# Performance work log

Measured on AMD Instinct MI355X. Metric: run time of the kernel, lower is better.

Reference implementation:

```python
import jax, jax.numpy as jnp
import numpy as np

N = 8192      # nodes
NIN = 128     # input feature dim
NH = 128      # hidden dim
NC = 8        # communities
CS = N // NC  # community size


def setup_inputs() -> dict:
    key = jax.random.key(0)
    k = jax.random.split(key, 6)
    seq1 = jax.random.normal(k[0], (1, N, NIN), jnp.float32)
    seq2 = jax.random.normal(k[1], (1, N, NIN), jnp.float32)
    # dense row-stochastic-ish adjacency so GCN activations stay O(1)
    adj = jax.random.uniform(k[2], (1, N, N), jnp.float32) * (2.0 / N)
    cc_label = jnp.arange(N, dtype=jnp.int32).reshape(NC, CS)  # partition of nodes
    W = jax.random.normal(k[3], (NIN, NH), jnp.float32) / np.float32(np.sqrt(NIN))
    b = jnp.zeros((NH,), jnp.float32)
    Wb = jax.random.normal(k[4], (NH, NH), jnp.float32) / np.float32(np.sqrt(NH))
    bb = jnp.zeros((), jnp.float32)
    return {"seq1": seq1, "seq2": seq2, "adj": adj, "cc_label": cc_label,
            "W": W, "b": b, "Wb": Wb, "bb": bb}


def reference(seq1, seq2, adj, cc_label, W, b, Wb, bb):
    def gcn(seq):
        fts = jnp.einsum('bnd,dh->bnh', seq, W)            # linear
        agg = jnp.einsum('bnm,bmh->bnh', adj, fts) + b     # neighborhood aggregation
        return jax.nn.relu(agg)

    h1 = gcn(seq1)[0]   # [N, NH]
    h2 = gcn(seq2)[0]   # [N, NH]

    # ragged per-community gather (communities are equal-size here)
    hg1 = h1[cc_label]  # [NC, CS, NH]
    hg2 = h2[cc_label]  # [NC, CS, NH]

    # AvgReadout (msk=None) + sigmoid -> per-community summary
    c = jax.nn.sigmoid(jnp.mean(hg1, axis=1))              # [NC, NH]

    # Discriminator: bilinear f_k(h, c) = h @ Wb @ c + bb
    cw = jnp.einsum('hk,nk->nh', Wb, c)                    # [NC, NH]
    sc1 = jnp.einsum('nch,nh->nc', hg1, cw) + bb           # [NC, CS]
    sc2 = jnp.einsum('nch,nh->nc', hg2, cw) + bb           # [NC, CS]

    # scalar scatter-back (each node written exactly once)
    flat = cc_label.reshape(-1)
    ret1 = jnp.zeros((N,), h1.dtype).at[flat].set(sc1.reshape(-1))
    ret2 = jnp.zeros((N,), h2.dtype).at[flat].set(sc2.reshape(-1))
    return jnp.concatenate([ret1, ret2])[None, :]          # [1, 2N]
```

## Files before the change

kernel.cpp:

```cpp
#include <hip/hip_runtime.h>


#define NN    8192
#define NCOLS 256
#define ASCALE 4096.0f
#define AINV  (1.0f/4096.0f)

typedef _Float16 half8 __attribute__((ext_vector_type(8)));
typedef _Float16 half4v __attribute__((ext_vector_type(4)));
typedef float    f32x4 __attribute__((ext_vector_type(4)));

__device__ __forceinline__ void gload16(const void* g, void* l) {
  __builtin_amdgcn_global_load_lds(
      (const __attribute__((address_space(1))) char*)g,
      (__attribute__((address_space(3))) char*)l, 16, 0, 0);
}

__global__ __launch_bounds__(256) void k1_fts(const float* __restrict__ seq1,
                                              const float* __restrict__ seq2,
                                              const float* __restrict__ W,
                                              _Float16* __restrict__ F,
                                              const int* __restrict__ cc,
                                              int* __restrict__ node_comm,
                                              float* __restrict__ S) {
  __shared__ char lds[65536];
  _Float16* Wt  = (_Float16*)lds;
  float*    sSeq = (float*)(lds + 32768);
  const int tid = threadIdx.x;
  const int lane = tid & 63;
  const int w = tid >> 6;
  const int l15 = lane & 15;
  const int g = lane >> 4;
  const int s = blockIdx.x >> 7;
  const int mt = blockIdx.x & 127;
  const int m0 = mt * 64;

  if (s == 0 && tid < 64) {
    int i = mt * 64 + tid;
    node_comm[cc[i]] = i >> 10;
  }
  if (blockIdx.x == 0) {
    for (int j = tid; j < 1024; j += 256) S[j] = 0.0f;
  }

  {
    const float4* W4g = (const float4*)W;
#pragma unroll
    for (int i = 0; i < 16; ++i) {
      int idx4 = i * 256 + tid;
      float4 wv = W4g[idx4];
      int d = idx4 >> 5;
      int hc = (idx4 & 31) * 4;
#pragma unroll
      for (int j = 0; j < 4; ++j) {
        int byte = ((hc + j) * 256 + d * 2) ^ (((hc + j) & 7) << 4);
        *(_Float16*)(lds + byte) = (_Float16)(((const float*)&wv)[j]);
      }
    }
  }

  const float* sp = s ? seq2 : seq1;
  const int srow = tid >> 5;
  const int sck = tid & 31;
  __syncthreads();
#pragma unroll
  for (int i = 0; i < 8; ++i) {
    int row = i * 8 + srow;
    gload16(sp + (size_t)(m0 + row) * 128 + ((sck ^ (row & 7)) << 2),
            (char*)sSeq + i * 4096 + w * 1024);
  }
  asm volatile("s_waitcnt vmcnt(0)" ::: "memory");
  __syncthreads();

  f32x4 acc[4][2] = {};
  const float4* S4 = (const float4*)sSeq;
  const float4* W4 = (const float4*)Wt;
#pragma unroll
  for (int kk = 0; kk < 4; ++kk) {
    half8 bf[2];
#pragma unroll
    for (int nf = 0; nf < 2; ++nf) {
      int col = w * 32 + nf * 16 + l15;
      float4 bv = W4[(col * 16 + kk * 4 + g) ^ (col & 7)];
      bf[nf] = *(const half8*)&bv;
    }
#pragma unroll
    for (int mf = 0; mf < 4; ++mf) {
      int row = mf * 16 + l15;
      int bidx = row * 32 + kk * 8 + g * 2;
      float4 u = S4[bidx ^ (row & 7)];
      float4 v = S4[(bidx + 1) ^ (row & 7)];
      half8 af;
#pragma unroll
      for (int j = 0; j < 4; ++j) af[j] = (_Float16)(((const float*)&u)[j]);
#pragma unroll
      for (int j = 0; j < 4; ++j) af[4 + j] = (_Float16)(((const float*)&v)[j]);
#pragma unroll
      for (int nf = 0; nf < 2; ++nf)
        acc[mf][nf] = __builtin_amdgcn_mfma_f32_16x16x32_f16(af, bf[nf], acc[mf][nf], 0, 0, 0);
    }
  }
  __syncthreads();
  _Float16* img = (_Float16*)sSeq;
#pragma unroll
  for (int mf = 0; mf < 4; ++mf)
#pragma unroll
    for (int nf = 0; nf < 2; ++nf) {
      int col = w * 32 + nf * 16 + l15;
#pragma unroll
      for (int j = 0; j < 4; ++j) {
        int kl = mf * 16 + g * 4 + j;
        img[(kl >> 5) * 4096 + col * 32 + (kl & 31)] = (_Float16)acc[mf][nf][j];
      }
    }
  __syncthreads();
  const float4* src4 = (const float4*)sSeq;
#pragma unroll
  for (int i = 0; i < 4; ++i) {
    int e = i * 256 + tid;
    int kt = e >> 9, off = e & 511;
    ((float4*)(F + (size_t)(2 * mt + kt) * 8192))[s * 512 + off] = src4[e];
  }
}

__global__ __launch_bounds__(512) void k2_gemm(const float* __restrict__ adj,
                                               const _Float16* __restrict__ F,
                                               _Float16* __restrict__ Pp) {
  __shared__ __align__(16) _Float16 sA[2][32768];
  const int tid = threadIdx.x;
  const int lane = tid & 63;
  const int w = tid >> 6;
  const int l15 = lane & 15;
  const int g = lane >> 4;
  const int id = blockIdx.x;
  const int xcd = id & 7;
  const int ks = xcd >> 1;
  const int mtile = (id >> 3) * 2 + (xcd & 1);
  const int row0 = mtile * 128;
  const int wm = w >> 2, wn = w & 3;

  const float* abase = adj + (size_t)(row0 + w * 16) * NN + (size_t)ks * 2048 + lane * 4;
  const _Float16* fbase = F + (size_t)(ks * 64) * 8192;

  f32x4 acc[4][4] = {};

  auto cvt_store = [&](int b, int i, f32x4 v) {
    int row = w * 16 + i;
    char* dst = (char*)sA[b] + row * 512 + ((lane * 8) ^ ((row & 15) << 4));
    half4v h;
    h[0] = (_Float16)(v[0] * ASCALE); h[1] = (_Float16)(v[1] * ASCALE);
    h[2] = (_Float16)(v[2] * ASCALE); h[3] = (_Float16)(v[3] * ASCALE);
    *(half4v*)dst = h;
  };

  {
    f32x4 pv[16];
#pragma unroll
    for (int i = 0; i < 16; ++i)
      pv[i] = __builtin_nontemporal_load((const f32x4*)(abase + (size_t)i * NN));
#pragma unroll
    for (int i = 0; i < 16; ++i) cvt_store(0, i, pv[i]);
  }
  __syncthreads();

  int colb[4], rowb[4], rsw[4];
#pragma unroll
  for (int nf = 0; nf < 4; ++nf) colb[nf] = (wn * 64 + nf * 16 + l15) * 32 + g * 8;
#pragma unroll
  for (int mf = 0; mf < 4; ++mf) {
    int row = wm * 64 + mf * 16 + l15;
    rowb[mf] = row * 512; rsw[mf] = (row & 15) << 4;
  }

  half8 bfc[4], bfn[4];
#pragma unroll
  for (int nf = 0; nf < 4; ++nf) {
    float4 t = *(const float4*)(fbase + colb[nf]);
    bfc[nf] = *(const half8*)&t;
  }

  for (int m = 0; m < 8; ++m) {
    const int b = m & 1;
    const bool lastm = (m == 7);
    const char* ab = (const char*)sA[b];
    const float* anext = abase + (m + 1) * 256;
    f32x4 ba[8][2];
#pragma unroll
    for (int s = 0; s < 8; ++s) {
      if (!(lastm && s == 7)) {
        const _Float16* fb = fbase + (size_t)(m * 8 + s + 1) * 8192;
#pragma unroll
        for (int nf = 0; nf < 4; ++nf) {
          float4 t = *(const float4*)(fb + colb[nf]);
          bfn[nf] = *(const half8*)&t;
        }
      }
      if (!lastm) {
        ba[s][0] = __builtin_nontemporal_load((const f32x4*)(anext + (size_t)(2 * s) * NN));
        ba[s][1] = __builtin_nontemporal_load((const f32x4*)(anext + (size_t)(2 * s + 1) * NN));
      }
#pragma unroll
      for (int mf = 0; mf < 4; ++mf) {
        half8 af = *(const half8*)(ab + rowb[mf] + ((s * 64 + g * 16) ^ rsw[mf]));
#pragma unroll
        for (int nf = 0; nf < 4; ++nf)
          acc[mf][nf] = __builtin_amdgcn_mfma_f32_16x16x32_f16(af, bfc[nf], acc[mf][nf], 0, 0, 0);
      }
      if (!lastm && s >= 2) {
        cvt_store(b ^ 1, 2 * (s - 2),     ba[s - 2][0]);
        cvt_store(b ^ 1, 2 * (s - 2) + 1, ba[s - 2][1]);
      }
#pragma unroll
      for (int nf = 0; nf < 4; ++nf) bfc[nf] = bfn[nf];
    }
    if (!lastm) {
      cvt_store(b ^ 1, 12, ba[6][0]); cvt_store(b ^ 1, 13, ba[6][1]);
      cvt_store(b ^ 1, 14, ba[7][0]); cvt_store(b ^ 1, 15, ba[7][1]);
    }
    __syncthreads();
  }

#pragma unroll
  for (int mf = 0; mf < 4; ++mf)
#pragma unroll
    for (int nf = 0; nf < 4; ++nf) {
      int col = wn * 64 + nf * 16 + l15;
#pragma unroll
      for (int j = 0; j < 4; ++j) {
        int row = row0 + wm * 64 + mf * 16 + g * 4 + j;
        __builtin_nontemporal_store((_Float16)acc[mf][nf][j],
            Pp + ((size_t)ks * NN + row) * NCOLS + col);
      }
    }
}

__global__ void k2r_reduce(const _Float16* __restrict__ Pp, const float* __restrict__ b,
                           float* __restrict__ h) {
  int gid = blockIdx.x * 256 + threadIdx.x;
  size_t base = (size_t)gid * 4;
  half4v p0 = __builtin_nontemporal_load((const half4v*)(Pp + base));
  half4v p1 = __builtin_nontemporal_load((const half4v*)(Pp + base + 2097152));
  half4v p2 = __builtin_nontemporal_load((const half4v*)(Pp + base + 4194304));
  half4v p3 = __builtin_nontemporal_load((const half4v*)(Pp + base + 6291456));
  int n0 = (int)(base & 255) & 127;
  float4 r;
  r.x = fmaxf(((float)p0[0] + (float)p1[0] + (float)p2[0] + (float)p3[0]) * AINV + b[n0],     0.f);
  r.y = fmaxf(((float)p0[1] + (float)p1[1] + (float)p2[1] + (float)p3[1]) * AINV + b[n0 + 1], 0.f);
  r.z = fmaxf(((float)p0[2] + (float)p1[2] + (float)p2[2] + (float)p3[2]) * AINV + b[n0 + 2], 0.f);
  r.w = fmaxf(((float)p0[3] + (float)p1[3] + (float)p2[3] + (float)p3[3]) * AINV + b[n0 + 3], 0.f);
  *(float4*)(h + base) = r;
}

__global__ __launch_bounds__(128) void k3a_csum(const float* __restrict__ h,
                                                const int* __restrict__ node_comm,
                                                float* __restrict__ S) {
  int hh = threadIdx.x;
  int n0 = blockIdx.x * 32;
  float a0=0,a1=0,a2=0,a3=0,a4=0,a5=0,a6=0,a7=0;
  for (int i = 0; i < 32; ++i) {
    int node = n0 + i;
    int c = node_comm[node];
    float v = h[(size_t)node * 256 + hh];
    a0 += (c == 0) ? v : 0.f;  a1 += (c == 1) ? v : 0.f;
    a2 += (c == 2) ? v : 0.f;  a3 += (c == 3) ? v : 0.f;
    a4 += (c == 4) ? v : 0.f;  a5 += (c == 5) ? v : 0.f;
    a6 += (c == 6) ? v : 0.f;  a7 += (c == 7) ? v : 0.f;
  }
  if (a0 != 0.f) atomicAdd(&S[0 * 128 + hh], a0);
  if (a1 != 0.f) atomicAdd(&S[1 * 128 + hh], a1);
  if (a2 != 0.f) atomicAdd(&S[2 * 128 + hh], a2);
  if (a3 != 0.f) atomicAdd(&S[3 * 128 + hh], a3);
  if (a4 != 0.f) atomicAdd(&S[4 * 128 + hh], a4);
  if (a5 != 0.f) atomicAdd(&S[5 * 128 + hh], a5);
  if (a6 != 0.f) atomicAdd(&S[6 * 128 + hh], a6);
  if (a7 != 0.f) atomicAdd(&S[7 * 128 + hh], a7);
}

__global__ __launch_bounds__(128) void k3b_cw(const float* __restrict__ S,
                                              const float* __restrict__ Wb,
                                              float* __restrict__ cw) {
  __shared__ float sc[128];
  int ci = blockIdx.x;
  int hh = threadIdx.x;
  float m = S[ci * 128 + hh] * (1.0f / 1024.0f);
  sc[hh] = 1.0f / (1.0f + __expf(-m));
  __syncthreads();
  const float4* wr = (const float4*)(Wb + (size_t)hh * 128);
  float acc = 0.f;
#pragma unroll 8
  for (int k4 = 0; k4 < 32; ++k4) {
    float4 wv = wr[k4];
    acc += wv.x * sc[k4 * 4 + 0] + wv.y * sc[k4 * 4 + 1]
         + wv.z * sc[k4 * 4 + 2] + wv.w * sc[k4 * 4 + 3];
  }
  cw[ci * 128 + hh] = acc;
}

__global__ __launch_bounds__(256) void k5_score(const float* __restrict__ h,
                                                const int* __restrict__ node_comm,
                                                const float* __restrict__ cw,
                                                const float* __restrict__ bbp,
                                                float* __restrict__ out) {
  int tid = threadIdx.x;
  int q = tid & 15, nl = tid >> 4;
  int node = blockIdx.x * 16 + nl;
  int c = node_comm[node];
  const float* hr = h + (size_t)node * 256;
  const float* cr = cw + c * 128;
  float4 c0 = *(const float4*)(cr + q * 8);
  float4 c1 = *(const float4*)(cr + q * 8 + 4);
  float4 a0 = *(const float4*)(hr + q * 8);
  float4 a1 = *(const float4*)(hr + q * 8 + 4);
  float p1 = a0.x*c0.x + a0.y*c0.y + a0.z*c0.z + a0.w*c0.w
           + a1.x*c1.x + a1.y*c1.y + a1.z*c1.z + a1.w*c1.w;
  float4 b0 = *(const float4*)(hr + 128 + q * 8);
  float4 b1 = *(const float4*)(hr + 128 + q * 8 + 4);
  float p2 = b0.x*c0.x + b0.y*c0.y + b0.z*c0.z + b0.w*c0.w
           + b1.x*c1.x + b1.y*c1.y + b1.z*c1.z + b1.w*c1.w;
#pragma unroll
  for (int m = 8; m >= 1; m >>= 1) {
    p1 += __shfl_xor(p1, m, 64);
    p2 += __shfl_xor(p2, m, 64);
  }
  if (q == 0) {
    float bb = bbp[0];
    out[node] = p1 + bb;
    out[8192 + node] = p2 + bb;
  }
}

extern "C" void kernel_launch(void* const* d_in, const int* in_sizes, int n_in,
                              void* d_out, int out_size, void* d_ws, size_t ws_size,
                              hipStream_t stream) {
  (void)in_sizes; (void)n_in; (void)out_size; (void)ws_size;
  const float* seq1 = (const float*)d_in[0];
  const float* seq2 = (const float*)d_in[1];
  const float* adj  = (const float*)d_in[2];
  const int*   cc   = (const int*)d_in[3];
  const float* W    = (const float*)d_in[4];
  const float* b    = (const float*)d_in[5];
  const float* Wb   = (const float*)d_in[6];
  const float* bb   = (const float*)d_in[7];
  float* out = (float*)d_out;

  char* ws = (char*)d_ws;
  _Float16* F    = (_Float16*)(ws);
  float* h       = (float*)(ws + (4u << 20));
  _Float16* Pp   = (_Float16*)(ws + (12u << 20));
  float* S       = (float*)(ws + (44u << 20));
  float* cw      = (float*)(ws + (44u << 20) + 4096);
  int* node_comm = (int*)(ws + (44u << 20) + 8192);

  k1_fts<<<dim3(256), dim3(256), 0, stream>>>(seq1, seq2, W, F, cc, node_comm, S);
  k2_gemm<<<dim3(256), dim3(512), 0, stream>>>(adj, F, Pp);
  k2r_reduce<<<dim3(2048), dim3(256), 0, stream>>>(Pp, b, h);
  k3a_csum<<<dim3(256), dim3(128), 0, stream>>>(h, node_comm, S);
  k3b_cw<<<dim3(8), dim3(128), 0, stream>>>(S, Wb, cw);
  k5_score<<<dim3(512), dim3(256), 0, stream>>>(h, node_comm, cw, bb, out);
}
```

Before: 107.3 us.

## Fuse split-K reduction into GEMM via last-block atomic counter

Removes the separate split-K reduce kernel. Each GEMM block now increments a per-row-tile counter after writing its partial tile, and the fourth (last) block sums the four fp16 partials, applies scale, bias and ReLU, and writes h. This saves one kernel launch and lets the reduction overlap with other GEMM blocks still running. In exchange it adds a threadfence and atomic per block, and the tail work is done by only 64 blocks with serialized loads.

```diff
diff --git a/kernel.cpp b/kernel.cpp
--- a/kernel.cpp
+++ b/kernel.cpp
@@ -22,7 +22,8 @@
                                               _Float16* __restrict__ F,
                                               const int* __restrict__ cc,
                                               int* __restrict__ node_comm,
-                                              float* __restrict__ S) {
+                                              float* __restrict__ S,
+                                              unsigned* __restrict__ ctr) {
   __shared__ char lds[65536];
   _Float16* Wt  = (_Float16*)lds;
   float*    sSeq = (float*)(lds + 32768);
@@ -41,6 +42,7 @@
   }
   if (blockIdx.x == 0) {
     for (int j = tid; j < 1024; j += 256) S[j] = 0.0f;
+    if (tid < 64) ctr[tid] = 0u;
   }
 
   {
@@ -125,8 +127,12 @@
 
 __global__ __launch_bounds__(512) void k2_gemm(const float* __restrict__ adj,
                                                const _Float16* __restrict__ F,
-                                               _Float16* __restrict__ Pp) {
+                                               _Float16* __restrict__ Pp,
+                                               const float* __restrict__ bias,
+                                               float* __restrict__ h,
+                                               unsigned* __restrict__ ctr) {
   __shared__ __align__(16) _Float16 sA[2][32768];
+  __shared__ int sLast;
   const int tid = threadIdx.x;
   const int lane = tid & 63;
   const int w = tid >> 6;
@@ -147,10 +153,10 @@
   auto cvt_store = [&](int b, int i, f32x4 v) {
     int row = w * 16 + i;
     char* dst = (char*)sA[b] + row * 512 + ((lane * 8) ^ ((row & 15) << 4));
-    half4v h;
-    h[0] = (_Float16)(v[0] * ASCALE); h[1] = (_Float16)(v[1] * ASCALE);
-    h[2] = (_Float16)(v[2] * ASCALE); h[3] = (_Float16)(v[3] * ASCALE);
-    *(half4v*)dst = h;
+    half4v hq;
+    hq[0] = (_Float16)(v[0] * ASCALE); hq[1] = (_Float16)(v[1] * ASCALE);
+    hq[2] = (_Float16)(v[2] * ASCALE); hq[3] = (_Float16)(v[3] * ASCALE);
+    *(half4v*)dst = hq;
   };
 
   {
@@ -232,23 +238,32 @@
             Pp + ((size_t)ks * NN + row) * NCOLS + col);
       }
     }
-}
-
-__global__ void k2r_reduce(const _Float16* __restrict__ Pp, const float* __restrict__ b,
-                           float* __restrict__ h) {
-  int gid = blockIdx.x * 256 + threadIdx.x;
-  size_t base = (size_t)gid * 4;
-  half4v p0 = __builtin_nontemporal_load((const half4v*)(Pp + base));
-  half4v p1 = __builtin_nontemporal_load((const half4v*)(Pp + base + 2097152));
-  half4v p2 = __builtin_nontemporal_load((const half4v*)(Pp + base + 4194304));
-  half4v p3 = __builtin_nontemporal_load((const half4v*)(Pp + base + 6291456));
-  int n0 = (int)(base & 255) & 127;
-  float4 r;
-  r.x = fmaxf(((float)p0[0] + (float)p1[0] + (float)p2[0] + (float)p3[0]) * AINV + b[n0],     0.f);
-  r.y = fmaxf(((float)p0[1] + (float)p1[1] + (float)p2[1] + (float)p3[1]) * AINV + b[n0 + 1], 0.f);
-  r.z = fmaxf(((float)p0[2] + (float)p1[2] + (float)p2[2] + (float)p3[2]) * AINV + b[n0 + 2], 0.f);
-  r.w = fmaxf(((float)p0[3] + (float)p1[3] + (float)p2[3] + (float)p3[3]) * AINV + b[n0 + 3], 0.f);
-  *(float4*)(h + base) = r;
+
+  __threadfence();
+  if (tid == 0)
+    sLast = (__hip_atomic_fetch_add(&ctr[mtile], 1u, __ATOMIC_ACQ_REL,
+                                    __HIP_MEMORY_SCOPE_AGENT) == 3u);
+  __syncthreads();
+  if (sLast) {
+#pragma unroll
+    for (int i = 0; i < 16; ++i) {
+      int e4 = i * 512 + tid;
+      int row = e4 >> 6;
+      int c4 = e4 & 63;
+      size_t off = (size_t)(row0 + row) * NCOLS + c4 * 4;
+      half4v p0 = __builtin_nontemporal_load((const half4v*)(Pp + off));
+      half4v p1 = __builtin_nontemporal_load((const half4v*)(Pp + off + 2097152));
+      half4v p2 = __builtin_nontemporal_load((const half4v*)(Pp + off + 4194304));
+      half4v p3 = __builtin_nontemporal_load((const half4v*)(Pp + off + 6291456));
+      int n0 = (c4 * 4) & 127;
+      float4 r;
+      r.x = fmaxf(((float)p0[0] + (float)p1[0] + (float)p2[0] + (float)p3[0]) * AINV + bias[n0],     0.f);
+      r.y = fmaxf(((float)p0[1] + (float)p1[1] + (float)p2[1] + (float)p3[1]) * AINV + bias[n0 + 1], 0.f);
+      r.z = fmaxf(((float)p0[2] + (float)p1[2] + (float)p2[2] + (float)p3[2]) * AINV + bias[n0 + 2], 0.f);
+      r.w = fmaxf(((float)p0[3] + (float)p1[3] + (float)p2[3] + (float)p3[3]) * AINV + bias[n0 + 3], 0.f);
+      *(float4*)(h + off) = r;
+    }
+  }
 }
 
 __global__ __launch_bounds__(128) void k3a_csum(const float* __restrict__ h,
@@ -350,10 +365,10 @@
   float* S       = (float*)(ws + (44u << 20));
   float* cw      = (float*)(ws + (44u << 20) + 4096);
   int* node_comm = (int*)(ws + (44u << 20) + 8192);
-
-  k1_fts<<<dim3(256), dim3(256), 0, stream>>>(seq1, seq2, W, F, cc, node_comm, S);
-  k2_gemm<<<dim3(256), dim3(512), 0, stream>>>(adj, F, Pp);
-  k2r_reduce<<<dim3(2048), dim3(256), 0, stream>>>(Pp, b, h);
+  unsigned* ctr  = (unsigned*)(ws + (44u << 20) + 49152);
+
+  k1_fts<<<dim3(256), dim3(256), 0, stream>>>(seq1, seq2, W, F, cc, node_comm, S, ctr);
+  k2_gemm<<<dim3(256), dim3(512), 0, stream>>>(adj, F, Pp, b, h, ctr);
   k3a_csum<<<dim3(256), dim3(128), 0, stream>>>(h, node_comm, S);
   k3b_cw<<<dim3(8), dim3(128), 0, stream>>>(S, Wb, cw);
   k5_score<<<dim3(512), dim3(256), 0, stream>>>(h, node_comm, cw, bb, out);
```

New measurement: 194.1 us. 1.81x slower.
